# Kernel tuning notes

Measured on AMD Instinct MI355X. Metric: run time of the kernel, lower is better.

## Reference

```python
import jax, jax.numpy as jnp
import numpy as np

N, L, D = 2048, 200, 64
NUM_USERS, NUM_ITEMS, NUM_R = 100000, 100000, 5


def _lin(x, W, b):
    # torch nn.Linear convention: W is [out, in]
    return x @ W.T + b


def setup_inputs() -> dict:
    key = jax.random.key(0)
    ks = jax.random.split(key, 12)
    s = 0.05
    return dict(
        nodes=jax.random.randint(ks[0], (N,), 0, NUM_ITEMS),
        history_uv=jax.random.randint(ks[1], (N, L), 0, NUM_USERS),
        history_r=jax.random.randint(ks[2], (N, L), 0, NUM_R),
        u2e=jax.random.normal(ks[3], (NUM_USERS, D), dtype=jnp.float32) * s,
        v2e=jax.random.normal(ks[4], (NUM_ITEMS, D), dtype=jnp.float32) * s,
        r2e=jax.random.normal(ks[5], (NUM_R, D), dtype=jnp.float32) * s,
        w_r1_w=jax.random.normal(ks[6], (D, 2 * D), dtype=jnp.float32) * s,
        w_r1_b=jnp.zeros((D,), jnp.float32),
        w_r2_w=jax.random.normal(ks[7], (D, D), dtype=jnp.float32) * s,
        w_r2_b=jnp.zeros((D,), jnp.float32),
        mu_w=jax.random.normal(ks[8], (D, 2 * D), dtype=jnp.float32) * s,
        mu_b=jnp.zeros((D,), jnp.float32),
        att1_w=jax.random.normal(ks[9], (D, 2 * D), dtype=jnp.float32) * s,
        att1_b=jnp.zeros((D,), jnp.float32),
        att2_w=jax.random.normal(ks[10], (D, D), dtype=jnp.float32) * s,
        att2_b=jnp.zeros((D,), jnp.float32),
        att3_w=jax.random.normal(ks[11], (1, D), dtype=jnp.float32) * s,
        att3_b=jnp.zeros((1,), jnp.float32),
    )


def reference(nodes, history_uv, history_r, u2e, v2e, r2e,
              w_r1_w, w_r1_b, w_r2_w, w_r2_b, mu_w, mu_b,
              att1_w, att1_b, att2_w, att2_b, att3_w, att3_b):
    # uv=False branch: neighbors are users, center nodes are items
    e_uv = u2e[history_uv]                     # [N, L, D]
    q = v2e[nodes]                             # [N, D]
    e_r = r2e[history_r]                       # [N, L, D]

    x = jax.nn.relu(_lin(jnp.concatenate([e_uv, e_r], -1), w_r1_w, w_r1_b))
    o = jax.nn.relu(_lin(x, w_r2_w, w_r2_b))   # [N, L, D]

    qb = jnp.broadcast_to(q[:, None, :], o.shape)   # [N, L, D]
    g = jax.nn.sigmoid(_lin(jnp.concatenate([o, qb], -1), mu_w, mu_b))
    o = g * o + (1.0 - g) * qb                 # gated history rep

    # Attention (dropout disabled / eval mode), softmax over the L neighbors
    a = jax.nn.relu(_lin(jnp.concatenate([o, qb], -1), att1_w, att1_b))
    a = jax.nn.relu(_lin(a, att2_w, att2_b))
    a = _lin(a, att3_w, att3_b)                # [N, L, 1]
    w = jax.nn.softmax(a, axis=1)

    return jnp.sum(w * o, axis=1)              # [N, D]
```

## Files before the change

kernel.cpp:

```cpp
#include <hip/hip_runtime.h>
#include <hip/hip_bf16.h>

typedef float f32x4 __attribute__((ext_vector_type(4)));
typedef __bf16 bf16x8 __attribute__((ext_vector_type(8)));

union Frag { unsigned short h[8]; unsigned int u[4]; uint4 u4; bf16x8 b; };

__device__ __forceinline__ unsigned short f2bs(float f){
  __hip_bfloat16 v = __float2bfloat16(f);
  return __builtin_bit_cast(unsigned short, v);
}
__device__ __forceinline__ unsigned int pk2(float a, float b){
  unsigned int r;
  asm("v_cvt_pk_bf16_f32 %0, %1, %2" : "=v"(r) : "v"(a), "v"(b));
  return r;
}
__device__ __forceinline__ Frag packF(f32x4 a, f32x4 b){
  Frag f;
  f.u[0] = pk2(a[0], a[1]); f.u[1] = pk2(a[2], a[3]);
  f.u[2] = pk2(b[0], b[1]); f.u[3] = pk2(b[2], b[3]);
  return f;
}
__device__ __forceinline__ f32x4 relu4(f32x4 v){
  f32x4 r;
  #pragma unroll
  for (int j = 0; j < 4; ++j) r[j] = fmaxf(v[j], 0.f);
  return r;
}
__device__ __forceinline__ float sigmoid_fast(float x){
  return __builtin_amdgcn_rcpf(1.f + __expf(-x));
}

__global__ void prep_weights(const float* __restrict__ w1, const float* __restrict__ w2,
                             const float* __restrict__ mu, const float* __restrict__ a1,
                             const float* __restrict__ a2, const float* __restrict__ r2e,
                             uint4* __restrict__ ws){
  const int f = blockIdx.x;
  const int l = threadIdx.x;
  Frag fr;
  if (f < 64){
    const float* W; int m, s, K;
    if (f < 16)      { W = w1; m = f >> 2;        s = f & 3;        K = 128; }
    else if (f < 24) { W = w2; m = (f - 16) >> 1; s = (f - 16) & 1; K = 64;  }
    else if (f < 40) { W = mu; m = (f - 24) >> 2; s = (f - 24) & 3; K = 128; }
    else if (f < 56) { W = a1; m = (f - 40) >> 2; s = (f - 40) & 3; K = 128; }
    else             { W = a2; m = (f - 56) >> 1; s = (f - 56) & 1; K = 64;  }
    const int row = 16 * m + (l & 15);
    const int k0  = 32 * s + 4 * (l >> 4);
    #pragma unroll
    for (int h = 0; h < 2; ++h)
      #pragma unroll
      for (int j = 0; j < 4; ++j)
        fr.h[4*h + j] = f2bs(W[row * K + k0 + 16*h + j]);
    ws[f * 64 + l] = fr.u4;
  } else {
    const int f2 = f - 64;
    const int R = f2 >> 1, sp = f2 & 1;
    const int g = (l >> 4) & 3;
    #pragma unroll
    for (int h = 0; h < 2; ++h)
      #pragma unroll
      for (int j = 0; j < 4; ++j)
        fr.h[4*h + j] = f2bs(r2e[R * 64 + sp * 32 + 16*h + 4*g + j]);
    ws[4096 + f2 * 64 + l] = fr.u4;
  }
}

__global__ __launch_bounds__(256)
void uv_agg_main(const int* __restrict__ nodes, const int* __restrict__ huv,
                 const int* __restrict__ hr, const float* __restrict__ u2e,
                 const float* __restrict__ v2e,
                 const float* __restrict__ b1g, const float* __restrict__ b2g,
                 const float* __restrict__ bmg, const float* __restrict__ ba1g,
                 const float* __restrict__ ba2g, const float* __restrict__ a3g,
                 const uint4* __restrict__ wsfrag, float* __restrict__ out){
  extern __shared__ unsigned char smem[];
  uint4* wlds = (uint4*)smem;
  float* bias = (float*)(smem + 65536);
  uint4* rlds = (uint4*)(smem + 67072);

  const int tid  = threadIdx.x;
  const int lane = tid & 63;
  const int wave = tid >> 6;
  const int g    = lane >> 4;
  const int r16  = lane & 15;
  const int n    = blockIdx.x * 4 + wave;

  #pragma unroll 4
  for (int i = tid; i < 4096; i += 256) wlds[i] = wsfrag[i];
  for (int i = tid; i < 640; i += 256)  rlds[i] = wsfrag[4096 + i];
  for (int i = tid; i < 384; i += 256){
    const int w = i >> 6, d = i & 63;
    const float* src = (w==0)?b1g:(w==1)?b2g:(w==2)?bmg:(w==3)?ba1g:(w==4)?ba2g:a3g;
    bias[i] = src[d];
  }
  __syncthreads();

  const uint4* wl = wlds + lane;
  const f32x4* bl = (const f32x4*)bias + g;
  const unsigned char* rbase = (const unsigned char*)rlds + lane * 16;
  const int* hu = huv + n * 200;
  const int* hrw = hr + n * 200;

  const int item = nodes[n];
  f32x4 qv[4];
  #pragma unroll
  for (int m = 0; m < 4; ++m)
    qv[m] = *(const f32x4*)(v2e + (size_t)item * 64 + 16*m + 4*g);
  Frag qf[2];
  qf[0] = packF(qv[0], qv[1]); qf[1] = packF(qv[2], qv[3]);

  float sw = 0.f;
  f32x4 accw[4];
  #pragma unroll
  for (int m = 0; m < 4; ++m) accw[m] = (f32x4)(0.f);

  int irA, irB;
  f32x4 urA[4], urB[4];
  {
    const int iuA = hu[r16];      irA = hrw[r16];
    const int iuB = hu[16 + r16]; irB = hrw[16 + r16];
    const f32x4* ua = (const f32x4*)(u2e + (size_t)iuA * 64);
    const f32x4* ub = (const f32x4*)(u2e + (size_t)iuB * 64);
    #pragma unroll
    for (int s = 0; s < 4; ++s){ urA[s] = ua[4*s + g]; urB[s] = ub[4*s + g]; }
  }

  for (int it = 0; it < 7; ++it){
    Frag b0A[2], b0B[2];
    b0A[0] = packF(urA[0], urA[1]); b0A[1] = packF(urA[2], urA[3]);
    b0B[0] = packF(urB[0], urB[1]); b0B[1] = packF(urB[2], urB[3]);
    const int ircA = irA, ircB = irB;
    const bool vA = (it < 6) || (r16 < 8);
    const bool vB = (it < 6);

    if (it < 6){
      const int base = (2*it + 2) * 16;
      const int kA = min(base + r16, 199);
      const int kB = min(base + 16 + r16, 199);
      const int iuA = hu[kA]; irA = hrw[kA];
      const int iuB = hu[kB]; irB = hrw[kB];
      const f32x4* ua = (const f32x4*)(u2e + (size_t)iuA * 64);
      const f32x4* ub = (const f32x4*)(u2e + (size_t)iuB * 64);
      #pragma unroll
      for (int s = 0; s < 4; ++s){ urA[s] = ua[4*s + g]; urB[s] = ub[4*s + g]; }
    }

    f32x4 XA[4], XB[4];
    #pragma unroll
    for (int m = 0; m < 4; ++m){
      const f32x4 bi = bl[0*16 + 4*m];
      f32x4 aA = bi, aB = bi;
      #pragma unroll
      for (int s = 0; s < 4; ++s){
        Frag w; w.u4 = wl[(m*4 + s) * 64];
        Frag eA, eB;
        if (s < 2){ eA = b0A[s]; eB = b0B[s]; }
        else {
          eA.u4 = *(const uint4*)(rbase + (size_t)(ircA*2 + (s-2)) * 1024);
          eB.u4 = *(const uint4*)(rbase + (size_t)(ircB*2 + (s-2)) * 1024);
        }
        aA = __builtin_amdgcn_mfma_f32_16x16x32_bf16(w.b, eA.b, aA, 0, 0, 0);
        aB = __builtin_amdgcn_mfma_f32_16x16x32_bf16(w.b, eB.b, aB, 0, 0, 0);
      }
      XA[m] = relu4(aA); XB[m] = relu4(aB);
    }
    Frag bxA[2], bxB[2];
    bxA[0] = packF(XA[0], XA[1]); bxA[1] = packF(XA[2], XA[3]);
    bxB[0] = packF(XB[0], XB[1]); bxB[1] = packF(XB[2], XB[3]);

    f32x4 OA[4], OB[4];
    #pragma unroll
    for (int m = 0; m < 4; ++m){
      const f32x4 bi = bl[1*16 + 4*m];
      f32x4 aA = bi, aB = bi;
      #pragma unroll
      for (int s = 0; s < 2; ++s){
        Frag w; w.u4 = wl[(16 + m*2 + s) * 64];
        aA = __builtin_amdgcn_mfma_f32_16x16x32_bf16(w.b, bxA[s].b, aA, 0, 0, 0);
        aB = __builtin_amdgcn_mfma_f32_16x16x32_bf16(w.b, bxB[s].b, aB, 0, 0, 0);
      }
      OA[m] = relu4(aA); OB[m] = relu4(aB);
    }
    Frag boA[2], boB[2];
    boA[0] = packF(OA[0], OA[1]); boA[1] = packF(OA[2], OA[3]);
    boB[0] = packF(OB[0], OB[1]); boB[1] = packF(OB[2], OB[3]);

    f32x4 OGA[4], OGB[4];
    #pragma unroll
    for (int m = 0; m < 4; ++m){
      const f32x4 bi = bl[2*16 + 4*m];
      f32x4 aA = bi, aB = bi;
      #pragma unroll
      for (int s = 0; s < 4; ++s){
        Frag w; w.u4 = wl[(24 + m*4 + s) * 64];
        const bf16x8 eA = (s < 2) ? boA[s].b : qf[s-2].b;
        const bf16x8 eB = (s < 2) ? boB[s].b : qf[s-2].b;
        aA = __builtin_amdgcn_mfma_f32_16x16x32_bf16(w.b, eA, aA, 0, 0, 0);
        aB = __builtin_amdgcn_mfma_f32_16x16x32_bf16(w.b, eB, aB, 0, 0, 0);
      }
      #pragma unroll
      for (int j = 0; j < 4; ++j){
        const float gA = sigmoid_fast(aA[j]);
        const float gB = sigmoid_fast(aB[j]);
        OGA[m][j] = fmaf(gA, OA[m][j] - qv[m][j], qv[m][j]);
        OGB[m][j] = fmaf(gB, OB[m][j] - qv[m][j], qv[m][j]);
      }
    }
    Frag bgA[2], bgB[2];
    bgA[0] = packF(OGA[0], OGA[1]); bgA[1] = packF(OGA[2], OGA[3]);
    bgB[0] = packF(OGB[0], OGB[1]); bgB[1] = packF(OGB[2], OGB[3]);

    f32x4 A1A[4], A1B[4];
    #pragma unroll
    for (int m = 0; m < 4; ++m){
      const f32x4 bi = bl[3*16 + 4*m];
      f32x4 aA = bi, aB = bi;
      #pragma unroll
      for (int s = 0; s < 4; ++s){
        Frag w; w.u4 = wl[(40 + m*4 + s) * 64];
        const bf16x8 eA = (s < 2) ? bgA[s].b : qf[s-2].b;
        const bf16x8 eB = (s < 2) ? bgB[s].b : qf[s-2].b;
        aA = __builtin_amdgcn_mfma_f32_16x16x32_bf16(w.b, eA, aA, 0, 0, 0);
        aB = __builtin_amdgcn_mfma_f32_16x16x32_bf16(w.b, eB, aB, 0, 0, 0);
      }
      A1A[m] = relu4(aA); A1B[m] = relu4(aB);
    }
    Frag b4A[2], b4B[2];
    b4A[0] = packF(A1A[0], A1A[1]); b4A[1] = packF(A1A[2], A1A[3]);
    b4B[0] = packF(A1B[0], A1B[1]); b4B[1] = packF(A1B[2], A1B[3]);

    float pA = 0.f, pB = 0.f;
    #pragma unroll
    for (int m = 0; m < 4; ++m){
      const f32x4 bi = bl[4*16 + 4*m];
      f32x4 aA = bi, aB = bi;
      #pragma unroll
      for (int s = 0; s < 2; ++s){
        Frag w; w.u4 = wl[(56 + m*2 + s) * 64];
        aA = __builtin_amdgcn_mfma_f32_16x16x32_bf16(w.b, b4A[s].b, aA, 0, 0, 0);
        aB = __builtin_amdgcn_mfma_f32_16x16x32_bf16(w.b, b4B[s].b, aB, 0, 0, 0);
      }
      aA = relu4(aA); aB = relu4(aB);
      const f32x4 a3m = bl[5*16 + 4*m];
      #pragma unroll
      for (int j = 0; j < 4; ++j){
        pA = fmaf(a3m[j], aA[j], pA);
        pB = fmaf(a3m[j], aB[j], pB);
      }
    }
    pA += __shfl_xor(pA, 16); pA += __shfl_xor(pA, 32);
    pB += __shfl_xor(pB, 16); pB += __shfl_xor(pB, 32);

    const float eA = vA ? __expf(fminf(pA, 60.f)) : 0.f;
    const float eB = vB ? __expf(fminf(pB, 60.f)) : 0.f;
    float esA = eA, esB = eB;
    #pragma unroll
    for (int o = 1; o < 16; o <<= 1){
      esA += __shfl_xor(esA, o);
      esB += __shfl_xor(esB, o);
    }
    sw += esA + esB;
    #pragma unroll
    for (int m = 0; m < 4; ++m)
      #pragma unroll
      for (int j = 0; j < 4; ++j)
        accw[m][j] = fmaf(eA, OGA[m][j], fmaf(eB, OGB[m][j], accw[m][j]));
  }

  #pragma unroll
  for (int m = 0; m < 4; ++m)
    #pragma unroll
    for (int j = 0; j < 4; ++j)
      #pragma unroll
      for (int o = 1; o < 16; o <<= 1)
        accw[m][j] += __shfl_xor(accw[m][j], o);
  if (r16 == 0){
    const float inv = 1.f / sw;
    #pragma unroll
    for (int m = 0; m < 4; ++m){
      f32x4 v = accw[m];
      #pragma unroll
      for (int j = 0; j < 4; ++j) v[j] *= inv;
      *(f32x4*)(out + (size_t)n * 64 + 16*m + 4*g) = v;
    }
  }
}

extern "C" void kernel_launch(void* const* d_in, const int* in_sizes, int n_in,
                              void* d_out, int out_size, void* d_ws, size_t ws_size,
                              hipStream_t stream){
  const int*   nodes = (const int*)  d_in[0];
  const int*   huv   = (const int*)  d_in[1];
  const int*   hr    = (const int*)  d_in[2];
  const float* u2e   = (const float*)d_in[3];
  const float* v2e   = (const float*)d_in[4];
  const float* r2e   = (const float*)d_in[5];
  const float* w1    = (const float*)d_in[6];
  const float* b1    = (const float*)d_in[7];
  const float* w2    = (const float*)d_in[8];
  const float* b2    = (const float*)d_in[9];
  const float* muw   = (const float*)d_in[10];
  const float* mub   = (const float*)d_in[11];
  const float* a1w   = (const float*)d_in[12];
  const float* a1b   = (const float*)d_in[13];
  const float* a2w   = (const float*)d_in[14];
  const float* a2b   = (const float*)d_in[15];
  const float* a3w   = (const float*)d_in[16];

  const int N = in_sizes[0];
  uint4* ws = (uint4*)d_ws;

  hipLaunchKernelGGL(prep_weights, dim3(74), dim3(64), 0, stream,
                     w1, w2, muw, a1w, a2w, r2e, ws);
  hipLaunchKernelGGL(uv_agg_main, dim3(N / 4), dim3(256), 77312, stream,
                     nodes, huv, hr, u2e, v2e,
                     b1, b2, mub, a1b, a2b, a3w,
                     (const uint4*)ws, (float*)d_out);
}
```

Baseline: 53.64 us.

## Split each node's history across two waves and merge partial softmax sums in LDS

Each block now runs 512 threads, and two waves share one node: one covers history chunks 0-3, the other chunks 4-6. Their unnormalized weighted sums and exp-sums are combined through shared memory before the final divide. The exp-sum reduction moves out of the loop into a single cross-lane reduction at the end. This doubles wave-level parallelism per node, which should cut the serial loop latency and help hide gather latency while amortizing the 64KB weight staging in LDS over more waves. The costs are a block-wide barrier, a little extra LDS, a tighter register budget under the 512-thread launch bound, and an uneven 4/3 chunk split between the two waves.

```diff
diff --git a/kernel.cpp b/kernel.cpp
--- a/kernel.cpp
+++ b/kernel.cpp
@@ -66,7 +66,7 @@
   }
 }
 
-__global__ __launch_bounds__(256)
+__global__ __launch_bounds__(512)
 void uv_agg_main(const int* __restrict__ nodes, const int* __restrict__ huv,
                  const int* __restrict__ hr, const float* __restrict__ u2e,
                  const float* __restrict__ v2e,
@@ -78,29 +78,33 @@
   uint4* wlds = (uint4*)smem;
   float* bias = (float*)(smem + 65536);
   uint4* rlds = (uint4*)(smem + 67072);
+  float* mAcc = (float*)(smem + 77312);
+  float* mSw  = (float*)(smem + 79360);
 
   const int tid  = threadIdx.x;
   const int lane = tid & 63;
   const int wave = tid >> 6;
+  const int ns   = wave & 3;
+  const int half = wave >> 2;
   const int g    = lane >> 4;
   const int r16  = lane & 15;
-  const int n    = blockIdx.x * 4 + wave;
-
-  #pragma unroll 4
-  for (int i = tid; i < 4096; i += 256) wlds[i] = wsfrag[i];
-  for (int i = tid; i < 640; i += 256)  rlds[i] = wsfrag[4096 + i];
-  for (int i = tid; i < 384; i += 256){
-    const int w = i >> 6, d = i & 63;
+  const int n    = blockIdx.x * 4 + ns;
+
+  #pragma unroll
+  for (int k = 0; k < 8; ++k) wlds[k * 512 + tid] = wsfrag[k * 512 + tid];
+  for (int i = tid; i < 640; i += 512)  rlds[i] = wsfrag[4096 + i];
+  if (tid < 384){
+    const int w = tid >> 6, d = tid & 63;
     const float* src = (w==0)?b1g:(w==1)?b2g:(w==2)?bmg:(w==3)?ba1g:(w==4)?ba2g:a3g;
-    bias[i] = src[d];
+    bias[tid] = src[d];
   }
   __syncthreads();
 
   const uint4* wl = wlds + lane;
   const f32x4* bl = (const f32x4*)bias + g;
   const unsigned char* rbase = (const unsigned char*)rlds + lane * 16;
-  const int* hu = huv + n * 200;
-  const int* hrw = hr + n * 200;
+  const int* hu  = huv + n * 200;
+  const int* hrw = hr  + n * 200;
 
   const int item = nodes[n];
   f32x4 qv[4];
@@ -110,32 +114,37 @@
   Frag qf[2];
   qf[0] = packF(qv[0], qv[1]); qf[1] = packF(qv[2], qv[3]);
 
-  float sw = 0.f;
+  float swl = 0.f;
   f32x4 accw[4];
   #pragma unroll
   for (int m = 0; m < 4; ++m) accw[m] = (f32x4)(0.f);
+
+  const int it0 = half ? 4 : 0;
+  const int itE = half ? 7 : 4;
 
   int irA, irB;
   f32x4 urA[4], urB[4];
   {
-    const int iuA = hu[r16];      irA = hrw[r16];
-    const int iuB = hu[16 + r16]; irB = hrw[16 + r16];
+    const int kA = min(32*it0 + r16, 199);
+    const int kB = min(32*it0 + 16 + r16, 199);
+    const int iuA = hu[kA]; irA = hrw[kA];
+    const int iuB = hu[kB]; irB = hrw[kB];
     const f32x4* ua = (const f32x4*)(u2e + (size_t)iuA * 64);
     const f32x4* ub = (const f32x4*)(u2e + (size_t)iuB * 64);
     #pragma unroll
     for (int s = 0; s < 4; ++s){ urA[s] = ua[4*s + g]; urB[s] = ub[4*s + g]; }
   }
 
-  for (int it = 0; it < 7; ++it){
+  for (int it = it0; it < itE; ++it){
     Frag b0A[2], b0B[2];
     b0A[0] = packF(urA[0], urA[1]); b0A[1] = packF(urA[2], urA[3]);
     b0B[0] = packF(urB[0], urB[1]); b0B[1] = packF(urB[2], urB[3]);
     const int ircA = irA, ircB = irB;
-    const bool vA = (it < 6) || (r16 < 8);
-    const bool vB = (it < 6);
-
-    if (it < 6){
-      const int base = (2*it + 2) * 16;
+    const bool vA = (32*it + r16) < 200;
+    const bool vB = (32*it + 16 + r16) < 200;
+
+    if (it + 1 < itE){
+      const int base = 32*it + 32;
       const int kA = min(base + r16, 199);
       const int kB = min(base + 16 + r16, 199);
       const int iuA = hu[kA]; irA = hrw[kA];
@@ -254,13 +263,7 @@
 
     const float eA = vA ? __expf(fminf(pA, 60.f)) : 0.f;
     const float eB = vB ? __expf(fminf(pB, 60.f)) : 0.f;
-    float esA = eA, esB = eB;
-    #pragma unroll
-    for (int o = 1; o < 16; o <<= 1){
-      esA += __shfl_xor(esA, o);
-      esB += __shfl_xor(esB, o);
-    }
-    sw += esA + esB;
+    swl += eA + eB;
     #pragma unroll
     for (int m = 0; m < 4; ++m)
       #pragma unroll
@@ -269,21 +272,27 @@
   }
 
   #pragma unroll
-  for (int m = 0; m < 4; ++m)
-    #pragma unroll
-    for (int j = 0; j < 4; ++j)
-      #pragma unroll
-      for (int o = 1; o < 16; o <<= 1)
+  for (int o = 1; o < 16; o <<= 1){
+    #pragma unroll
+    for (int m = 0; m < 4; ++m)
+      #pragma unroll
+      for (int j = 0; j < 4; ++j)
         accw[m][j] += __shfl_xor(accw[m][j], o);
+    swl += __shfl_xor(swl, o);
+  }
   if (r16 == 0){
-    const float inv = 1.f / sw;
-    #pragma unroll
-    for (int m = 0; m < 4; ++m){
-      f32x4 v = accw[m];
-      #pragma unroll
-      for (int j = 0; j < 4; ++j) v[j] *= inv;
-      *(f32x4*)(out + (size_t)n * 64 + 16*m + 4*g) = v;
-    }
+    float* dst = mAcc + (ns * 2 + half) * 64;
+    #pragma unroll
+    for (int m = 0; m < 4; ++m)
+      *(f32x4*)(dst + 16*m + 4*g) = accw[m];
+    if (lane == 0) mSw[ns * 2 + half] = swl;
+  }
+  __syncthreads();
+  if (tid < 256){
+    const int n2 = tid >> 6, d = tid & 63;
+    const float tot = mSw[n2 * 2] + mSw[n2 * 2 + 1];
+    const float v = (mAcc[n2 * 128 + d] + mAcc[n2 * 128 + 64 + d]) / tot;
+    out[(size_t)(blockIdx.x * 4 + n2) * 64 + d] = v;
   }
 }
 
@@ -313,7 +322,7 @@
 
   hipLaunchKernelGGL(prep_weights, dim3(74), dim3(64), 0, stream,
                      w1, w2, muw, a1w, a2w, r2e, ws);
-  hipLaunchKernelGGL(uv_agg_main, dim3(N / 4), dim3(256), 77312, stream,
+  hipLaunchKernelGGL(uv_agg_main, dim3(N / 4), dim3(512), 79392, stream,
                      nodes, huv, hr, u2e, v2e,
                      b1, b2, mub, a1b, a2b, a3w,
                      (const uint4*)ws, (float*)d_out);
```

Result: slower. 56.04 us (+4.5%).

## Read weight fragments from global memory instead of staging them in LDS

Applied to the files above, without the earlier changes.

Drops the 64KB weight-fragment copy into shared memory. MFMA weight fragments are now read straight from the global workspace, where L2/L1 caching is expected to serve them. LDS use falls to about 11KB per block, which allows more resident blocks per CU and removes the per-block 64KB staging load. The per-iteration softmax-denominator shuffle reduction is also deferred into the final cross-lane reduction. In exchange, every MFMA weight load now goes through the vector memory path and may add latency.

```diff
diff --git a/kernel.cpp b/kernel.cpp
--- a/kernel.cpp
+++ b/kernel.cpp
@@ -74,10 +74,8 @@
                  const float* __restrict__ bmg, const float* __restrict__ ba1g,
                  const float* __restrict__ ba2g, const float* __restrict__ a3g,
                  const uint4* __restrict__ wsfrag, float* __restrict__ out){
-  extern __shared__ unsigned char smem[];
-  uint4* wlds = (uint4*)smem;
-  float* bias = (float*)(smem + 65536);
-  uint4* rlds = (uint4*)(smem + 67072);
+  __shared__ float bias[384];
+  __shared__ uint4 rlds[640];
 
   const int tid  = threadIdx.x;
   const int lane = tid & 63;
@@ -86,21 +84,19 @@
   const int r16  = lane & 15;
   const int n    = blockIdx.x * 4 + wave;
 
-  #pragma unroll 4
-  for (int i = tid; i < 4096; i += 256) wlds[i] = wsfrag[i];
   for (int i = tid; i < 640; i += 256)  rlds[i] = wsfrag[4096 + i];
-  for (int i = tid; i < 384; i += 256){
-    const int w = i >> 6, d = i & 63;
+  if (tid < 384){
+    const int w = tid >> 6, d = tid & 63;
     const float* src = (w==0)?b1g:(w==1)?b2g:(w==2)?bmg:(w==3)?ba1g:(w==4)?ba2g:a3g;
-    bias[i] = src[d];
+    bias[tid] = src[d];
   }
   __syncthreads();
 
-  const uint4* wl = wlds + lane;
+  const uint4* wl = wsfrag + lane;
   const f32x4* bl = (const f32x4*)bias + g;
   const unsigned char* rbase = (const unsigned char*)rlds + lane * 16;
-  const int* hu = huv + n * 200;
-  const int* hrw = hr + n * 200;
+  const int* hu  = huv + n * 200;
+  const int* hrw = hr  + n * 200;
 
   const int item = nodes[n];
   f32x4 qv[4];
@@ -110,7 +106,7 @@
   Frag qf[2];
   qf[0] = packF(qv[0], qv[1]); qf[1] = packF(qv[2], qv[3]);
 
-  float sw = 0.f;
+  float swl = 0.f;
   f32x4 accw[4];
   #pragma unroll
   for (int m = 0; m < 4; ++m) accw[m] = (f32x4)(0.f);
@@ -131,11 +127,11 @@
     b0A[0] = packF(urA[0], urA[1]); b0A[1] = packF(urA[2], urA[3]);
     b0B[0] = packF(urB[0], urB[1]); b0B[1] = packF(urB[2], urB[3]);
     const int ircA = irA, ircB = irB;
-    const bool vA = (it < 6) || (r16 < 8);
-    const bool vB = (it < 6);
+    const bool vA = (32*it + r16) < 200;
+    const bool vB = (32*it + 16 + r16) < 200;
 
     if (it < 6){
-      const int base = (2*it + 2) * 16;
+      const int base = 32*it + 32;
       const int kA = min(base + r16, 199);
       const int kB = min(base + 16 + r16, 199);
       const int iuA = hu[kA]; irA = hrw[kA];
@@ -254,13 +250,7 @@
 
     const float eA = vA ? __expf(fminf(pA, 60.f)) : 0.f;
     const float eB = vB ? __expf(fminf(pB, 60.f)) : 0.f;
-    float esA = eA, esB = eB;
-    #pragma unroll
-    for (int o = 1; o < 16; o <<= 1){
-      esA += __shfl_xor(esA, o);
-      esB += __shfl_xor(esB, o);
-    }
-    sw += esA + esB;
+    swl += eA + eB;
     #pragma unroll
     for (int m = 0; m < 4; ++m)
       #pragma unroll
@@ -269,14 +259,16 @@
   }
 
   #pragma unroll
-  for (int m = 0; m < 4; ++m)
-    #pragma unroll
-    for (int j = 0; j < 4; ++j)
-      #pragma unroll
-      for (int o = 1; o < 16; o <<= 1)
+  for (int o = 1; o < 16; o <<= 1){
+    #pragma unroll
+    for (int m = 0; m < 4; ++m)
+      #pragma unroll
+      for (int j = 0; j < 4; ++j)
         accw[m][j] += __shfl_xor(accw[m][j], o);
+    swl += __shfl_xor(swl, o);
+  }
   if (r16 == 0){
-    const float inv = 1.f / sw;
+    const float inv = 1.f / swl;
     #pragma unroll
     for (int m = 0; m < 4; ++m){
       f32x4 v = accw[m];
@@ -313,7 +305,7 @@
 
   hipLaunchKernelGGL(prep_weights, dim3(74), dim3(64), 0, stream,
                      w1, w2, muw, a1w, a2w, r2e, ws);
-  hipLaunchKernelGGL(uv_agg_main, dim3(N / 4), dim3(256), 77312, stream,
+  hipLaunchKernelGGL(uv_agg_main, dim3(N / 4), dim3(256), 0, stream,
                      nodes, huv, hr, u2e, v2e,
                      b1, b2, mub, a1b, a2b, a3w,
                      (const uint4*)ws, (float*)d_out);
```

After: 146.2 us. 2.72x slower.
